# Kernel tuning notes

Hardware: AMD Instinct MI355X
Metric: run time of the kernel (lower is better)

## Reference

```python
import jax, jax.numpy as jnp
import numpy as np

B, K, U, I, D = 16384, 64, 100000, 100000, 256

def setup_inputs() -> dict:
    key = jax.random.key(0)
    k1, k2, k3, k4, k5, k6, k7, k8 = jax.random.split(key, 8)
    return {
        "nodes_u": jax.random.randint(k1, (B,), 0, U),
        "nodes_v": jax.random.randint(k2, (B,), 0, I),
        "neighbors": jax.random.randint(k3, (B, K), 0, U),
        "neighbor_counts": jax.random.randint(k4, (B,), 0, K + 1),
        "u2e": jax.random.normal(k5, (U, D), dtype=jnp.float32),
        "v2e": jax.random.normal(k6, (I, D), dtype=jnp.float32),
        "W": jax.random.normal(k7, (D, 2 * D), dtype=jnp.float32) * 0.05,  # torch Linear weight [out, in]
        "b": jax.random.normal(k8, (D,), dtype=jnp.float32) * 0.05,
    }

def reference(nodes_u, nodes_v, neighbors, neighbor_counts, u2e, v2e, W, b):
    # self embeddings [B, D]
    self_emb = u2e[nodes_u]
    # gather padded neighbor embeddings [B, K, D]
    neib_emb = u2e[neighbors]
    k_ = neighbors.shape[1]
    mask = jnp.arange(k_)[None, :] < neighbor_counts[:, None]          # [B, K] valid-neighbor mask
    nsum = jnp.einsum('bkd,bk->bd', neib_emb, mask.astype(neib_emb.dtype))
    cnt = jnp.maximum(neighbor_counts, 1).astype(self_emb.dtype)[:, None]
    nmean = nsum / cnt                                                  # mean-pool over valid neighbors
    cat = jnp.concatenate([self_emb, nmean], axis=1)                    # [B, 2D]
    proj = cat @ W.T + b                                                # Linear(2D -> D)
    # users with no neighbors use raw self embedding (matches `if len(neibs) > 0` branch)
    uemb = jnp.where((neighbor_counts > 0)[:, None], proj, self_emb)
    scores = jnp.sum(uemb * v2e[nodes_v], axis=1)                       # [B]
    return scores
```

## Files before the change

kernel.cpp:

```cpp
#include <hip/hip_runtime.h>

#define B_ROWS   16384
#define K_NB     64
#define D_DIM    256
#define TWO_D    512
#define R_BLK    8
#define THREADS  256

__global__ __launch_bounds__(THREADS)
void easyrec_fused(const int* __restrict__ nodes_u,
                   const int* __restrict__ nodes_v,
                   const int* __restrict__ neighbors,
                   const int* __restrict__ neighbor_counts,
                   const float* __restrict__ u2e,
                   const float* __restrict__ v2e,
                   const float* __restrict__ W,
                   const float* __restrict__ bias,
                   float* __restrict__ out)
{
    __shared__ __align__(16) int nbr_lds[R_BLK * K_NB];
    __shared__ __align__(16) float cat_lds[R_BLK][TWO_D];
    __shared__ float red_lds[R_BLK * 4];
    __shared__ float selfdot_lds[R_BLK];
    __shared__ float bdot_lds[R_BLK];

    const int t    = threadIdx.x;
    const int wave = t >> 6;
    const int lane = t & 63;
    const int row0 = blockIdx.x * R_BLK;

    nbr_lds[t]           = neighbors[(size_t)row0 * K_NB + t];
    nbr_lds[t + THREADS] = neighbors[(size_t)row0 * K_NB + t + THREADS];
    __syncthreads();

    for (int rr = 0; rr < 2; ++rr) {
        const int r   = wave + rr * 4;
        const int row = row0 + r;
        const int nu  = __builtin_amdgcn_readfirstlane(nodes_u[row]);
        const int nv  = __builtin_amdgcn_readfirstlane(nodes_v[row]);
        const int cnt = __builtin_amdgcn_readfirstlane(neighbor_counts[row]);

        const float4 self4 = *(const float4*)(u2e + (size_t)nu * D_DIM + 4 * lane);
        const float4 v4    = *(const float4*)(v2e + (size_t)nv * D_DIM + 4 * lane);
        const float4 b4    = *(const float4*)(bias + 4 * lane);

        float4 acc = make_float4(0.f, 0.f, 0.f, 0.f);
        const int base = r * K_NB;
        const int kmax = (cnt + 7) & ~7;
        for (int k = 0; k < kmax; k += 8) {
            const int4 ia = *(const int4*)&nbr_lds[base + k];
            const int4 ib = *(const int4*)&nbr_lds[base + k + 4];
            const float4 n0 = *(const float4*)(u2e + (size_t)ia.x * D_DIM + 4 * lane);
            const float4 n1 = *(const float4*)(u2e + (size_t)ia.y * D_DIM + 4 * lane);
            const float4 n2 = *(const float4*)(u2e + (size_t)ia.z * D_DIM + 4 * lane);
            const float4 n3 = *(const float4*)(u2e + (size_t)ia.w * D_DIM + 4 * lane);
            const float4 n4 = *(const float4*)(u2e + (size_t)ib.x * D_DIM + 4 * lane);
            const float4 n5 = *(const float4*)(u2e + (size_t)ib.y * D_DIM + 4 * lane);
            const float4 n6 = *(const float4*)(u2e + (size_t)ib.z * D_DIM + 4 * lane);
            const float4 n7 = *(const float4*)(u2e + (size_t)ib.w * D_DIM + 4 * lane);
            if (k + 8 <= cnt) {
                acc.x += n0.x + n1.x + n2.x + n3.x + n4.x + n5.x + n6.x + n7.x;
                acc.y += n0.y + n1.y + n2.y + n3.y + n4.y + n5.y + n6.y + n7.y;
                acc.z += n0.z + n1.z + n2.z + n3.z + n4.z + n5.z + n6.z + n7.z;
                acc.w += n0.w + n1.w + n2.w + n3.w + n4.w + n5.w + n6.w + n7.w;
            } else {
                const float m0 = (k + 0 < cnt) ? 1.f : 0.f;
                const float m1 = (k + 1 < cnt) ? 1.f : 0.f;
                const float m2 = (k + 2 < cnt) ? 1.f : 0.f;
                const float m3 = (k + 3 < cnt) ? 1.f : 0.f;
                const float m4 = (k + 4 < cnt) ? 1.f : 0.f;
                const float m5 = (k + 5 < cnt) ? 1.f : 0.f;
                const float m6 = (k + 6 < cnt) ? 1.f : 0.f;
                const float m7 = (k + 7 < cnt) ? 1.f : 0.f;
                acc.x += n0.x*m0 + n1.x*m1 + n2.x*m2 + n3.x*m3 + n4.x*m4 + n5.x*m5 + n6.x*m6 + n7.x*m7;
                acc.y += n0.y*m0 + n1.y*m1 + n2.y*m2 + n3.y*m3 + n4.y*m4 + n5.y*m5 + n6.y*m6 + n7.y*m7;
                acc.z += n0.z*m0 + n1.z*m1 + n2.z*m2 + n3.z*m3 + n4.z*m4 + n5.z*m5 + n6.z*m6 + n7.z*m7;
                acc.w += n0.w*m0 + n1.w*m1 + n2.w*m2 + n3.w*m3 + n4.w*m4 + n5.w*m5 + n6.w*m6 + n7.w*m7;
            }
        }
        const float inv = 1.0f / (float)(cnt > 0 ? cnt : 1);
        float4 nm = make_float4(acc.x * inv, acc.y * inv, acc.z * inv, acc.w * inv);

        *(float4*)(&cat_lds[r][4 * lane])         = self4;
        *(float4*)(&cat_lds[r][D_DIM + 4 * lane]) = nm;

        float sv = self4.x * v4.x + self4.y * v4.y + self4.z * v4.z + self4.w * v4.w;
        float bv = b4.x * v4.x + b4.y * v4.y + b4.z * v4.z + b4.w * v4.w;
        #pragma unroll
        for (int off = 32; off > 0; off >>= 1) {
            sv += __shfl_xor(sv, off, 64);
            bv += __shfl_xor(bv, off, 64);
        }
        if (lane == 0) { selfdot_lds[r] = sv; bdot_lds[r] = bv; }
    }
    __syncthreads();

    const float* vrow[R_BLK];
    #pragma unroll
    for (int r = 0; r < R_BLK; ++r) {
        const int nv = __builtin_amdgcn_readfirstlane(nodes_v[row0 + r]);
        vrow[r] = v2e + (size_t)nv * D_DIM;
    }

    float2 acc2[R_BLK];
    #pragma unroll
    for (int r = 0; r < R_BLK; ++r) acc2[r] = make_float2(0.f, 0.f);

    for (int d = 0; d < D_DIM; d += 4) {
        float4 vq[R_BLK];
        #pragma unroll
        for (int r = 0; r < R_BLK; ++r) vq[r] = *(const float4*)(vrow[r] + d);

        #pragma unroll
        for (int dd = 0; dd < 4; ++dd) {
            const float2 wq = *(const float2*)(W + (size_t)(d + dd) * TWO_D + 2 * t);
            #pragma unroll
            for (int r = 0; r < R_BLK; ++r) {
                const float vs = (dd == 0) ? vq[r].x : (dd == 1) ? vq[r].y
                               : (dd == 2) ? vq[r].z : vq[r].w;
                acc2[r].x += wq.x * vs;
                acc2[r].y += wq.y * vs;
            }
        }
    }

    #pragma unroll
    for (int r = 0; r < R_BLK; ++r) {
        const float2 c2 = *(const float2*)(&cat_lds[r][2 * t]);
        float p = c2.x * acc2[r].x + c2.y * acc2[r].y;
        #pragma unroll
        for (int off = 32; off > 0; off >>= 1) p += __shfl_xor(p, off, 64);
        if (lane == 0) red_lds[r * 4 + wave] = p;
    }
    __syncthreads();

    if (t < R_BLK) {
        const int row = row0 + t;
        const int cnt = neighbor_counts[row];
        float s;
        if (cnt > 0) {
            s = red_lds[t * 4 + 0] + red_lds[t * 4 + 1]
              + red_lds[t * 4 + 2] + red_lds[t * 4 + 3] + bdot_lds[t];
        } else {
            s = selfdot_lds[t];
        }
        out[row] = s;
    }
}

extern "C" void kernel_launch(void* const* d_in, const int* in_sizes, int n_in,
                              void* d_out, int out_size, void* d_ws, size_t ws_size,
                              hipStream_t stream) {
    const int*   nodes_u         = (const int*)d_in[0];
    const int*   nodes_v         = (const int*)d_in[1];
    const int*   neighbors       = (const int*)d_in[2];
    const int*   neighbor_counts = (const int*)d_in[3];
    const float* u2e             = (const float*)d_in[4];
    const float* v2e             = (const float*)d_in[5];
    const float* W               = (const float*)d_in[6];
    const float* bias            = (const float*)d_in[7];
    float*       out             = (float*)d_out;

    const int blocks = B_ROWS / R_BLK;
    easyrec_fused<<<blocks, THREADS, 0, stream>>>(
        nodes_u, nodes_v, neighbors, neighbor_counts, u2e, v2e, W, bias, out);
}
```

Before: 320.1 us.

## Interleave neighbor gathers for two rows per wave and use 32-bit offsets

Restructures the neighbor mean-pool so each wave gathers neighbors for both of its rows in the same loop iteration, doubling the independent gather loads in flight before accumulation, then finishes the longer row in a tail loop. Address arithmetic switches from 64-bit size_t indexing to 32-bit byte offsets with shifts, and launch bounds now request 4 blocks per CU. The aim is to hide gather latency and cut address-computation instructions. It risks higher register pressure from two sets of eight float4 loads, and the tail loop now always multiplies by masks.

```diff
diff --git a/kernel.cpp b/kernel.cpp
--- a/kernel.cpp
+++ b/kernel.cpp
@@ -7,7 +7,7 @@
 #define R_BLK    8
 #define THREADS  256
 
-__global__ __launch_bounds__(THREADS)
+__global__ __launch_bounds__(THREADS, 4)
 void easyrec_fused(const int* __restrict__ nodes_u,
                    const int* __restrict__ nodes_v,
                    const int* __restrict__ neighbors,
@@ -18,7 +18,7 @@
                    const float* __restrict__ bias,
                    float* __restrict__ out)
 {
-    __shared__ __align__(16) int nbr_lds[R_BLK * K_NB];
+    __shared__ __align__(16) int   nbr_lds[R_BLK * K_NB];
     __shared__ __align__(16) float cat_lds[R_BLK][TWO_D];
     __shared__ float red_lds[R_BLK * 4];
     __shared__ float selfdot_lds[R_BLK];
@@ -33,87 +33,132 @@
     nbr_lds[t + THREADS] = neighbors[(size_t)row0 * K_NB + t + THREADS];
     __syncthreads();
 
-    for (int rr = 0; rr < 2; ++rr) {
-        const int r   = wave + rr * 4;
-        const int row = row0 + r;
-        const int nu  = __builtin_amdgcn_readfirstlane(nodes_u[row]);
-        const int nv  = __builtin_amdgcn_readfirstlane(nodes_v[row]);
-        const int cnt = __builtin_amdgcn_readfirstlane(neighbor_counts[row]);
-
-        const float4 self4 = *(const float4*)(u2e + (size_t)nu * D_DIM + 4 * lane);
-        const float4 v4    = *(const float4*)(v2e + (size_t)nv * D_DIM + 4 * lane);
-        const float4 b4    = *(const float4*)(bias + 4 * lane);
-
-        float4 acc = make_float4(0.f, 0.f, 0.f, 0.f);
-        const int base = r * K_NB;
-        const int kmax = (cnt + 7) & ~7;
-        for (int k = 0; k < kmax; k += 8) {
-            const int4 ia = *(const int4*)&nbr_lds[base + k];
-            const int4 ib = *(const int4*)&nbr_lds[base + k + 4];
-            const float4 n0 = *(const float4*)(u2e + (size_t)ia.x * D_DIM + 4 * lane);
-            const float4 n1 = *(const float4*)(u2e + (size_t)ia.y * D_DIM + 4 * lane);
-            const float4 n2 = *(const float4*)(u2e + (size_t)ia.z * D_DIM + 4 * lane);
-            const float4 n3 = *(const float4*)(u2e + (size_t)ia.w * D_DIM + 4 * lane);
-            const float4 n4 = *(const float4*)(u2e + (size_t)ib.x * D_DIM + 4 * lane);
-            const float4 n5 = *(const float4*)(u2e + (size_t)ib.y * D_DIM + 4 * lane);
-            const float4 n6 = *(const float4*)(u2e + (size_t)ib.z * D_DIM + 4 * lane);
-            const float4 n7 = *(const float4*)(u2e + (size_t)ib.w * D_DIM + 4 * lane);
-            if (k + 8 <= cnt) {
-                acc.x += n0.x + n1.x + n2.x + n3.x + n4.x + n5.x + n6.x + n7.x;
-                acc.y += n0.y + n1.y + n2.y + n3.y + n4.y + n5.y + n6.y + n7.y;
-                acc.z += n0.z + n1.z + n2.z + n3.z + n4.z + n5.z + n6.z + n7.z;
-                acc.w += n0.w + n1.w + n2.w + n3.w + n4.w + n5.w + n6.w + n7.w;
-            } else {
-                const float m0 = (k + 0 < cnt) ? 1.f : 0.f;
-                const float m1 = (k + 1 < cnt) ? 1.f : 0.f;
-                const float m2 = (k + 2 < cnt) ? 1.f : 0.f;
-                const float m3 = (k + 3 < cnt) ? 1.f : 0.f;
-                const float m4 = (k + 4 < cnt) ? 1.f : 0.f;
-                const float m5 = (k + 5 < cnt) ? 1.f : 0.f;
-                const float m6 = (k + 6 < cnt) ? 1.f : 0.f;
-                const float m7 = (k + 7 < cnt) ? 1.f : 0.f;
-                acc.x += n0.x*m0 + n1.x*m1 + n2.x*m2 + n3.x*m3 + n4.x*m4 + n5.x*m5 + n6.x*m6 + n7.x*m7;
-                acc.y += n0.y*m0 + n1.y*m1 + n2.y*m2 + n3.y*m3 + n4.y*m4 + n5.y*m5 + n6.y*m6 + n7.y*m7;
-                acc.z += n0.z*m0 + n1.z*m1 + n2.z*m2 + n3.z*m3 + n4.z*m4 + n5.z*m5 + n6.z*m6 + n7.z*m7;
-                acc.w += n0.w*m0 + n1.w*m1 + n2.w*m2 + n3.w*m3 + n4.w*m4 + n5.w*m5 + n6.w*m6 + n7.w*m7;
+    const unsigned colb = (unsigned)lane * 16u;
+
+    {
+        const float4 b4 = *(const float4*)((const char*)bias + colb);
+        #pragma unroll
+        for (int rr = 0; rr < 2; ++rr) {
+            const int r   = wave + rr * 4;
+            const int row = row0 + r;
+            const int nu  = __builtin_amdgcn_readfirstlane(nodes_u[row]);
+            const int nv  = __builtin_amdgcn_readfirstlane(nodes_v[row]);
+            const float4 self4 = *(const float4*)((const char*)u2e + (((unsigned)nu) << 10) + colb);
+            const float4 v4    = *(const float4*)((const char*)v2e + (((unsigned)nv) << 10) + colb);
+            *(float4*)(&cat_lds[r][4 * lane]) = self4;
+            float sv = self4.x * v4.x + self4.y * v4.y + self4.z * v4.z + self4.w * v4.w;
+            float bv = b4.x * v4.x + b4.y * v4.y + b4.z * v4.z + b4.w * v4.w;
+            #pragma unroll
+            for (int off = 32; off > 0; off >>= 1) {
+                sv += __shfl_xor(sv, off, 64);
+                bv += __shfl_xor(bv, off, 64);
             }
-        }
-        const float inv = 1.0f / (float)(cnt > 0 ? cnt : 1);
-        float4 nm = make_float4(acc.x * inv, acc.y * inv, acc.z * inv, acc.w * inv);
-
-        *(float4*)(&cat_lds[r][4 * lane])         = self4;
-        *(float4*)(&cat_lds[r][D_DIM + 4 * lane]) = nm;
-
-        float sv = self4.x * v4.x + self4.y * v4.y + self4.z * v4.z + self4.w * v4.w;
-        float bv = b4.x * v4.x + b4.y * v4.y + b4.z * v4.z + b4.w * v4.w;
-        #pragma unroll
-        for (int off = 32; off > 0; off >>= 1) {
-            sv += __shfl_xor(sv, off, 64);
-            bv += __shfl_xor(bv, off, 64);
-        }
-        if (lane == 0) { selfdot_lds[r] = sv; bdot_lds[r] = bv; }
+            if (lane == 0) { selfdot_lds[r] = sv; bdot_lds[r] = bv; }
+        }
+    }
+
+    const int rowA = row0 + wave, rowB = rowA + 4;
+    const int cntA = __builtin_amdgcn_readfirstlane(neighbor_counts[rowA]);
+    const int cntB = __builtin_amdgcn_readfirstlane(neighbor_counts[rowB]);
+    const int itA = (cntA + 7) >> 3;
+    const int itB = (cntB + 7) >> 3;
+    const int itMin = itA < itB ? itA : itB;
+    const int itMax = itA > itB ? itA : itB;
+    const int baseA = wave * K_NB;
+    const int baseB = baseA + 4 * K_NB;
+
+#define LOAD8(P, BASE, KK)                                                          \
+    const int4 P##ia = *(const int4*)&nbr_lds[(BASE) + (KK)];                       \
+    const int4 P##ib = *(const int4*)&nbr_lds[(BASE) + (KK) + 4];                   \
+    const float4 P##n0 = *(const float4*)((const char*)u2e + (((unsigned)P##ia.x) << 10) + colb); \
+    const float4 P##n1 = *(const float4*)((const char*)u2e + (((unsigned)P##ia.y) << 10) + colb); \
+    const float4 P##n2 = *(const float4*)((const char*)u2e + (((unsigned)P##ia.z) << 10) + colb); \
+    const float4 P##n3 = *(const float4*)((const char*)u2e + (((unsigned)P##ia.w) << 10) + colb); \
+    const float4 P##n4 = *(const float4*)((const char*)u2e + (((unsigned)P##ib.x) << 10) + colb); \
+    const float4 P##n5 = *(const float4*)((const char*)u2e + (((unsigned)P##ib.y) << 10) + colb); \
+    const float4 P##n6 = *(const float4*)((const char*)u2e + (((unsigned)P##ib.z) << 10) + colb); \
+    const float4 P##n7 = *(const float4*)((const char*)u2e + (((unsigned)P##ib.w) << 10) + colb);
+
+#define ACC8(P, ACC, CNT, KK)                                                       \
+    {                                                                               \
+        const float m0 = ((KK) + 0 < (CNT)) ? 1.f : 0.f;                            \
+        const float m1 = ((KK) + 1 < (CNT)) ? 1.f : 0.f;                            \
+        const float m2 = ((KK) + 2 < (CNT)) ? 1.f : 0.f;                            \
+        const float m3 = ((KK) + 3 < (CNT)) ? 1.f : 0.f;                            \
+        const float m4 = ((KK) + 4 < (CNT)) ? 1.f : 0.f;                            \
+        const float m5 = ((KK) + 5 < (CNT)) ? 1.f : 0.f;                            \
+        const float m6 = ((KK) + 6 < (CNT)) ? 1.f : 0.f;                            \
+        const float m7 = ((KK) + 7 < (CNT)) ? 1.f : 0.f;                            \
+        ACC.x += m0*P##n0.x + m1*P##n1.x + m2*P##n2.x + m3*P##n3.x                  \
+               + m4*P##n4.x + m5*P##n5.x + m6*P##n6.x + m7*P##n7.x;                 \
+        ACC.y += m0*P##n0.y + m1*P##n1.y + m2*P##n2.y + m3*P##n3.y                  \
+               + m4*P##n4.y + m5*P##n5.y + m6*P##n6.y + m7*P##n7.y;                 \
+        ACC.z += m0*P##n0.z + m1*P##n1.z + m2*P##n2.z + m3*P##n3.z                  \
+               + m4*P##n4.z + m5*P##n5.z + m6*P##n6.z + m7*P##n7.z;                 \
+        ACC.w += m0*P##n0.w + m1*P##n1.w + m2*P##n2.w + m3*P##n3.w                  \
+               + m4*P##n4.w + m5*P##n5.w + m6*P##n6.w + m7*P##n7.w;                 \
+    }
+
+    float4 accA = make_float4(0.f, 0.f, 0.f, 0.f);
+    float4 accB = make_float4(0.f, 0.f, 0.f, 0.f);
+
+    for (int i = 0; i < itMin; ++i) {
+        const int k = i << 3;
+        LOAD8(A, baseA, k)
+        LOAD8(B, baseB, k)
+        ACC8(A, accA, cntA, k)
+        ACC8(B, accB, cntB, k)
+    }
+    if (itMin < itMax) {
+        const bool Along = itA > itB;
+        const int  cntL  = Along ? cntA : cntB;
+        const int  baseL = Along ? baseA : baseB;
+        float4 accL = make_float4(0.f, 0.f, 0.f, 0.f);
+        for (int i = itMin; i < itMax; ++i) {
+            const int k = i << 3;
+            LOAD8(L, baseL, k)
+            ACC8(L, accL, cntL, k)
+        }
+        if (Along) {
+            accA.x += accL.x; accA.y += accL.y; accA.z += accL.z; accA.w += accL.w;
+        } else {
+            accB.x += accL.x; accB.y += accL.y; accB.z += accL.z; accB.w += accL.w;
+        }
+    }
+#undef LOAD8
+#undef ACC8
+
+    {
+        const float invA = 1.0f / (float)(cntA > 0 ? cntA : 1);
+        const float invB = 1.0f / (float)(cntB > 0 ? cntB : 1);
+        *(float4*)(&cat_lds[wave][D_DIM + 4 * lane]) =
+            make_float4(accA.x * invA, accA.y * invA, accA.z * invA, accA.w * invA);
+        *(float4*)(&cat_lds[wave + 4][D_DIM + 4 * lane]) =
+            make_float4(accB.x * invB, accB.y * invB, accB.z * invB, accB.w * invB);
     }
     __syncthreads();
 
-    const float* vrow[R_BLK];
+    unsigned voff[R_BLK];
     #pragma unroll
     for (int r = 0; r < R_BLK; ++r) {
         const int nv = __builtin_amdgcn_readfirstlane(nodes_v[row0 + r]);
-        vrow[r] = v2e + (size_t)nv * D_DIM;
+        voff[r] = ((unsigned)nv) << 10;
     }
 
     float2 acc2[R_BLK];
     #pragma unroll
     for (int r = 0; r < R_BLK; ++r) acc2[r] = make_float2(0.f, 0.f);
 
+    const unsigned tb8 = (unsigned)t * 8u;
     for (int d = 0; d < D_DIM; d += 4) {
         float4 vq[R_BLK];
         #pragma unroll
-        for (int r = 0; r < R_BLK; ++r) vq[r] = *(const float4*)(vrow[r] + d);
+        for (int r = 0; r < R_BLK; ++r)
+            vq[r] = *(const float4*)((const char*)v2e + voff[r] + (unsigned)d * 4u);
 
         #pragma unroll
         for (int dd = 0; dd < 4; ++dd) {
-            const float2 wq = *(const float2*)(W + (size_t)(d + dd) * TWO_D + 2 * t);
+            const float2 wq = *(const float2*)((const char*)W + (((unsigned)(d + dd)) << 11) + tb8);
             #pragma unroll
             for (int r = 0; r < R_BLK; ++r) {
                 const float vs = (dd == 0) ? vq[r].x : (dd == 1) ? vq[r].y
```

Measured after the change: 327.3 us. 2.2% more time.
